# Kernel optimization log

Measured on AMD Instinct MI355X. Metric: run time of the kernel, lower is better.

## Reference

```python
import jax, jax.numpy as jnp
import numpy as np


def _log_g(x):
    # log of g(x) = where(x>=0, x+0.5, sigmoid(x)), computed stably in log space
    return jnp.where(x >= 0.0, jnp.log(jax.nn.relu(x) + 0.5), -jax.nn.softplus(-x))


def setup_inputs() -> dict:
    key = jax.random.key(0)
    k1, k2, k3, k4 = jax.random.split(key, 4)
    B, T, D, H = 4, 8192, 512, 512
    x = jax.random.normal(k1, (B, T, D), dtype=jnp.float32)
    h_prev = jax.random.uniform(k2, (B, 1, H), dtype=jnp.float32)  # positive: log(h0) taken
    W_h = jax.random.normal(k3, (H, D), dtype=jnp.float32) * (1.0 / np.sqrt(D))
    b_h = jnp.zeros((H,), dtype=jnp.float32)
    W_z = jax.random.normal(k4, (H, D), dtype=jnp.float32) * (1.0 / np.sqrt(D))
    b_z = jnp.zeros((H,), dtype=jnp.float32)
    return {"x": x, "h_prev": h_prev, "W_h": W_h, "b_h": b_h, "W_z": W_z, "b_z": b_z}


def reference(x, h_prev, W_h, b_h, W_z, b_z):
    # parallel (seq_len > 1) minGRU forward via Heinsen log-space scan
    k = jnp.einsum('btd,hd->bth', x, W_z) + b_z           # (B,T,H) gate pre-activation
    log_z = -jax.nn.softplus(-k)                          # log sigmoid(k)
    log_coeffs = -jax.nn.softplus(k)                      # log (1 - sigmoid(k))
    log_tilde_h = _log_g(jnp.einsum('btd,hd->bth', x, W_h) + b_h)
    log_h0 = jnp.log(h_prev)                              # (B,1,H)
    log_values = jnp.concatenate([log_h0, log_z + log_tilde_h], axis=1)  # (B,T+1,H)
    # a_star = [0, cumsum(log_coeffs)]
    a_star = jnp.pad(jnp.cumsum(log_coeffs, axis=1), ((0, 0), (1, 0), (0, 0)))
    log_h = a_star + jax.lax.cumlogsumexp(log_values - a_star, axis=1)
    h = jnp.exp(log_h)[:, 1:]                             # drop h0 -> (B,T,H)
    return h
```

## Files before the change

### kernel.cpp

```cpp
#include <hip/hip_runtime.h>
#include <hip/hip_bf16.h>
#include <stdint.h>

#define B_ 4
#define T_ 8192
#define D_ 512
#define H_ 512
#define M_ (B_ * T_)
#define SEG 32
#define SPB 256
#define NSEG (M_ / SEG)

typedef __attribute__((ext_vector_type(8))) short short8;
typedef __attribute__((ext_vector_type(4))) float floatx4;
typedef __attribute__((ext_vector_type(2))) float float2e;

__device__ __forceinline__ unsigned short f2bf(float f) {
    union { float f; unsigned int u; } v; v.f = f;
    unsigned int u = v.u;
    u += 0x7fffu + ((u >> 16) & 1u);
    return (unsigned short)(u >> 16);
}
__device__ __forceinline__ float bf_lo(unsigned int u) {
    union { unsigned int i; float f; } a; a.i = u << 16; return a.f;
}
__device__ __forceinline__ float bf_hi(unsigned int u) {
    union { unsigned int i; float f; } a; a.i = u & 0xffff0000u; return a.f;
}
__device__ __forceinline__ unsigned int pk_cd(float c, float d) {
    return (unsigned int)f2bf(c) | ((unsigned int)f2bf(d) << 16);
}

#define X8 (M_ * D_ / 8)
#define W8 (H_ * D_ / 8)

__global__ __launch_bounds__(256)
void conv_all(const float* __restrict__ x,
              const float* __restrict__ Wz,
              const float* __restrict__ Wh,
              unsigned short* __restrict__ xbf,
              unsigned short* __restrict__ Wf)
{
    const int gid    = blockIdx.x * blockDim.x + threadIdx.x;
    const int stride = gridDim.x * blockDim.x;
    for (int i = gid; i < X8; i += stride) {
        floatx4 a = __builtin_nontemporal_load((const floatx4*)x + 2 * i);
        floatx4 b = __builtin_nontemporal_load((const floatx4*)x + 2 * i + 1);
        short8 w;
        w[0] = (short)f2bf(a[0]); w[1] = (short)f2bf(a[1]);
        w[2] = (short)f2bf(a[2]); w[3] = (short)f2bf(a[3]);
        w[4] = (short)f2bf(b[0]); w[5] = (short)f2bf(b[1]);
        w[6] = (short)f2bf(b[2]); w[7] = (short)f2bf(b[3]);
        *((short8*)xbf + i) = w;
    }
    if (gid < 2 * W8) {
        const int i = gid;
        const float* src = (i < W8) ? Wz : Wh;
        const int idx = (i < W8) ? i : i - W8;
        floatx4 a = __builtin_nontemporal_load((const floatx4*)src + 2 * idx);
        floatx4 b = __builtin_nontemporal_load((const floatx4*)src + 2 * idx + 1);
        short8 w;
        w[0] = (short)f2bf(a[0]); w[1] = (short)f2bf(a[1]);
        w[2] = (short)f2bf(a[2]); w[3] = (short)f2bf(a[3]);
        w[4] = (short)f2bf(b[0]); w[5] = (short)f2bf(b[1]);
        w[6] = (short)f2bf(b[2]); w[7] = (short)f2bf(b[3]);
        *((short8*)Wf + i) = w;
    }
}

#define LDSB 32768

__global__ __launch_bounds__(256, 4)
void gemm_cd(const unsigned short* __restrict__ xbf,
             const unsigned short* __restrict__ Wf,
             const float* __restrict__ bz, const float* __restrict__ bh,
             unsigned int* __restrict__ cd,
             float2* __restrict__ Sagg)
{
    __shared__ __align__(16) char smem[LDSB];
    unsigned short* lds = (unsigned short*)smem;
    unsigned int*   cdl = (unsigned int*)smem;

    const int tid  = threadIdx.x;
    const int lane = tid & 63;
    const int wave = tid >> 6;
    const int xcd  = blockIdx.x & 7;
    const int nblk = (blockIdx.x >> 3) & 7;
    const int mblk = xcd * 32 + (blockIdx.x >> 6);
    const int m0 = mblk * 128;
    const int n0 = nblk * 64;
    const int wm = (wave >> 1) * 64;
    const int wn = (wave & 1) * 32;
    const int l15  = lane & 15;
    const int quad = lane >> 4;
    const int srow = lane >> 2;
    const int sp   = lane & 3;

    #define STAGE(p, kt)                                                          \
    {                                                                             \
        const int kb = (kt) * 32;                                                 \
        unsigned short* bb = lds + (p) * 8192;                                    \
        _Pragma("unroll")                                                         \
        for (int r = 0; r < 2; ++r) {                                             \
            const int chunk = r * 4 + wave;                                       \
            const int row   = chunk * 16 + srow;                                  \
            const int kp    = sp ^ (row & 3);                                     \
            __builtin_amdgcn_global_load_lds(                                     \
                (const __attribute__((address_space(1))) unsigned int*)           \
                    (xbf + (size_t)(m0 + row) * D_ + kb + kp * 8),                \
                (__attribute__((address_space(3))) unsigned int*)(bb + chunk * 512),\
                16, 0, 0);                                                        \
        }                                                                         \
        {                                                                         \
            const int row = wave * 16 + srow;                                     \
            const int kp  = sp ^ (row & 3);                                       \
            __builtin_amdgcn_global_load_lds(                                     \
                (const __attribute__((address_space(1))) unsigned int*)           \
                    (Wf + (size_t)(n0 + row) * D_ + kb + kp * 8),                 \
                (__attribute__((address_space(3))) unsigned int*)(bb + 4096 + wave * 512),\
                16, 0, 0);                                                        \
            __builtin_amdgcn_global_load_lds(                                     \
                (const __attribute__((address_space(1))) unsigned int*)           \
                    (Wf + (size_t)(512 + n0 + row) * D_ + kb + kp * 8),           \
                (__attribute__((address_space(3))) unsigned int*)(bb + 6144 + wave * 512),\
                16, 0, 0);                                                        \
        }                                                                         \
    }

    floatx4 acc_z[4][2], acc_h[4][2];
    #pragma unroll
    for (int i = 0; i < 4; ++i)
        #pragma unroll
        for (int j = 0; j < 2; ++j) { acc_z[i][j] = (floatx4)0.0f; acc_h[i][j] = (floatx4)0.0f; }

    STAGE(0, 0);

    for (int kt = 0; kt < 16; ++kt) {
        __syncthreads();
        const int base = (kt & 1) * 8192;
        short8 af[4], zf[2], hf[2];
        #pragma unroll
        for (int i = 0; i < 4; ++i) {
            const int ra = wm + i * 16 + l15;
            af[i] = *(const short8*)&lds[base + ra * 32 + ((quad ^ (ra & 3)) * 8)];
        }
        #pragma unroll
        for (int j = 0; j < 2; ++j) {
            const int rb = wn + j * 16 + l15;
            zf[j] = *(const short8*)&lds[base + 4096 + rb * 32 + ((quad ^ (rb & 3)) * 8)];
            hf[j] = *(const short8*)&lds[base + 6144 + rb * 32 + ((quad ^ (rb & 3)) * 8)];
        }
        if (kt < 15) STAGE((kt + 1) & 1, kt + 1);
        #pragma unroll
        for (int i = 0; i < 4; ++i)
            #pragma unroll
            for (int j = 0; j < 2; ++j) {
                acc_z[i][j] = __builtin_amdgcn_mfma_f32_16x16x32_bf16(zf[j], af[i], acc_z[i][j], 0, 0, 0);
                acc_h[i][j] = __builtin_amdgcn_mfma_f32_16x16x32_bf16(hf[j], af[i], acc_h[i][j], 0, 0, 0);
            }
    }

    __syncthreads();

    #pragma unroll
    for (int j = 0; j < 2; ++j) {
        const int hlb = wn + j * 16 + quad * 4;
        const float4 bzv = *(const float4*)&bz[n0 + hlb];
        const float4 bhv = *(const float4*)&bh[n0 + hlb];
        #pragma unroll
        for (int i = 0; i < 4; ++i) {
            const int mloc = wm + i * 16 + l15;
            uint4 w;
            #pragma unroll
            for (int r = 0; r < 4; ++r) {
                float kz = acc_z[i][j][r] + ((const float*)&bzv)[r];
                float hp = acc_h[i][j][r] + ((const float*)&bhv)[r];
                float c  = 1.0f / (1.0f + __expf(kz));
                float g  = (hp >= 0.0f) ? (hp + 0.5f) : (1.0f / (1.0f + __expf(-hp)));
                float d  = (1.0f - c) * g;
                ((unsigned int*)&w)[r] = pk_cd(c, d);
            }
            *(uint4*)&cd[(size_t)(m0 + mloc) * H_ + n0 + hlb] = w;
            *(uint4*)&cdl[mloc * 64 + (hlb ^ ((mloc & 7) << 2))] = w;
        }
    }

    __syncthreads();

    {
        float C = 1.0f, Dv = 0.0f;
        const int t0 = wave * 32;
        #pragma unroll
        for (int t = 0; t < 32; ++t) {
            const int row = t0 + t;
            unsigned int u = cdl[row * 64 + (lane ^ ((row & 7) << 2))];
            float c = bf_lo(u), d = bf_hi(u);
            Dv = fmaf(c, Dv, d);
            C *= c;
        }
        const int chain = (m0 >> 13) * 512 + n0 + lane;
        const int seg   = ((m0 >> 5) & 255) + wave;
        Sagg[(size_t)chain * SPB + seg] = make_float2(C, Dv);
    }
    #undef STAGE
}

__global__ __launch_bounds__(256)
void interseg(const float* __restrict__ h_prev,
              const float2* __restrict__ Sagg,
              float* __restrict__ Hseg)
{
    const int chain = blockIdx.x * 4 + (threadIdx.x >> 6);
    const int lane  = threadIdx.x & 63;
    const float2* spp = Sagg + (size_t)chain * SPB + lane * 4;
    float4 q0 = *(const float4*)&spp[0];
    float4 q1 = *(const float4*)&spp[2];
    float C = q0.x, D = q0.y;
    D = fmaf(q0.z, D, q0.w);  C *= q0.z;
    D = fmaf(q1.x, D, q1.y);  C *= q1.x;
    D = fmaf(q1.z, D, q1.w);  C *= q1.z;
    #pragma unroll
    for (int off = 1; off < 64; off <<= 1) {
        float Cp = __shfl_up(C, off, 64);
        float Dp = __shfl_up(D, off, 64);
        if (lane >= off) { D = fmaf(C, Dp, D); C *= Cp; }
    }
    float Ce = __shfl_up(C, 1, 64);
    float De = __shfl_up(D, 1, 64);
    if (lane == 0) { Ce = 1.0f; De = 0.0f; }
    const float h0 = h_prev[chain];
    float hs = fmaf(Ce, h0, De);
    float4 o;
    o.x = hs;
    hs = fmaf(q0.x, hs, q0.y); o.y = hs;
    hs = fmaf(q0.z, hs, q0.w); o.z = hs;
    hs = fmaf(q1.x, hs, q1.y); o.w = hs;
    *(float4*)&Hseg[(size_t)chain * SPB + lane * 4] = o;
}

__global__ __launch_bounds__(256)
void apply_scan(const unsigned int* __restrict__ cd,
                const float* __restrict__ Hseg,
                float* __restrict__ out)
{
    const int sg = blockIdx.x;
    const int b  = sg >> 8;
    const int s  = sg & 255;
    const int h  = threadIdx.x * 2;
    const unsigned int* base = cd + (size_t)sg * SEG * H_ + h;
    float* ob = out + (size_t)sg * SEG * H_ + h;
    uint2 v[SEG];
    #pragma unroll
    for (int t = 0; t < SEG; ++t)
        v[t] = *(const uint2*)(base + (size_t)t * H_);
    float hs0 = Hseg[(size_t)(b * 512 + h)     * SPB + s];
    float hs1 = Hseg[(size_t)(b * 512 + h + 1) * SPB + s];
    #pragma unroll
    for (int t = 0; t < SEG; ++t) {
        hs0 = fmaf(bf_lo(v[t].x), hs0, bf_hi(v[t].x));
        hs1 = fmaf(bf_lo(v[t].y), hs1, bf_hi(v[t].y));
        float2e o; o.x = hs0; o.y = hs1;
        __builtin_nontemporal_store(o, (float2e*)(ob + (size_t)t * H_));
    }
}

extern "C" void kernel_launch(void* const* d_in, const int* in_sizes, int n_in,
                              void* d_out, int out_size, void* d_ws, size_t ws_size,
                              hipStream_t stream)
{
    const float* x      = (const float*)d_in[0];
    const float* h_prev = (const float*)d_in[1];
    const float* W_h    = (const float*)d_in[2];
    const float* b_h    = (const float*)d_in[3];
    const float* W_z    = (const float*)d_in[4];
    const float* b_z    = (const float*)d_in[5];
    float* out = (float*)d_out;

    unsigned short* xbf = (unsigned short*)d_out;

    char* ws = (char*)d_ws;
    unsigned int* cd = (unsigned int*)ws;
    size_t cd_bytes = (size_t)M_ * H_ * 4;
    unsigned short* Wf = (unsigned short*)(ws + cd_bytes);
    size_t wf_bytes = (size_t)2 * H_ * D_ * sizeof(unsigned short);
    float2* Sagg = (float2*)(ws + cd_bytes + wf_bytes);
    float*  Hseg = (float*)((char*)Sagg + (size_t)2048 * SPB * sizeof(float2));

    conv_all<<<dim3(2048), dim3(256), 0, stream>>>(x, W_z, W_h, xbf, Wf);
    gemm_cd<<<dim3((M_ / 128) * (H_ / 64)), dim3(256), 0, stream>>>(
        xbf, Wf, b_z, b_h, cd, Sagg);
    interseg<<<dim3(512), dim3(256), 0, stream>>>(h_prev, Sagg, Hseg);
    apply_scan<<<dim3(NSEG), dim3(256), 0, stream>>>(cd, Hseg, out);
}
```

Before: 197.9 us.

## Triple-buffer GEMM K-loop, add nontemporal stores, widen apply_scan to 4 channels

The GEMM main loop moves from double to triple buffering in LDS, keeping two stages in flight. It replaces __syncthreads with explicit vmcnt waits and s_barrier, and unrolls the loop fully. The larger LDS footprint lowers the occupancy bound from 4 to 3 blocks. Stores of cd, Sagg and Hseg become nontemporal, and apply_scan now handles 4 channels per thread with 128-bit loads and stores, two segments per block, streaming loads instead of preloading all 32 rows into registers.

```diff
diff --git a/kernel.cpp b/kernel.cpp
--- a/kernel.cpp
+++ b/kernel.cpp
@@ -14,6 +14,7 @@
 typedef __attribute__((ext_vector_type(8))) short short8;
 typedef __attribute__((ext_vector_type(4))) float floatx4;
 typedef __attribute__((ext_vector_type(2))) float float2e;
+typedef __attribute__((ext_vector_type(4))) unsigned int uintx4;
 
 __device__ __forceinline__ unsigned short f2bf(float f) {
     union { float f; unsigned int u; } v; v.f = f;
@@ -68,9 +69,9 @@
     }
 }
 
-#define LDSB 32768
-
-__global__ __launch_bounds__(256, 4)
+#define LDSB 49152
+
+__global__ __launch_bounds__(256, 3)
 void gemm_cd(const unsigned short* __restrict__ xbf,
              const unsigned short* __restrict__ Wf,
              const float* __restrict__ bz, const float* __restrict__ bh,
@@ -134,10 +135,15 @@
         for (int j = 0; j < 2; ++j) { acc_z[i][j] = (floatx4)0.0f; acc_h[i][j] = (floatx4)0.0f; }
 
     STAGE(0, 0);
-
+    STAGE(1, 1);
+    __builtin_amdgcn_sched_barrier(0);
+    asm volatile("s_waitcnt vmcnt(4)" ::: "memory");
+    __builtin_amdgcn_s_barrier();
+    __builtin_amdgcn_sched_barrier(0);
+
+    #pragma unroll
     for (int kt = 0; kt < 16; ++kt) {
-        __syncthreads();
-        const int base = (kt & 1) * 8192;
+        const int base = (kt % 3) * 8192;
         short8 af[4], zf[2], hf[2];
         #pragma unroll
         for (int i = 0; i < 4; ++i) {
@@ -150,7 +156,7 @@
             zf[j] = *(const short8*)&lds[base + 4096 + rb * 32 + ((quad ^ (rb & 3)) * 8)];
             hf[j] = *(const short8*)&lds[base + 6144 + rb * 32 + ((quad ^ (rb & 3)) * 8)];
         }
-        if (kt < 15) STAGE((kt + 1) & 1, kt + 1);
+        if (kt <= 13) STAGE((kt + 2) % 3, kt + 2);
         #pragma unroll
         for (int i = 0; i < 4; ++i)
             #pragma unroll
@@ -158,6 +164,13 @@
                 acc_z[i][j] = __builtin_amdgcn_mfma_f32_16x16x32_bf16(zf[j], af[i], acc_z[i][j], 0, 0, 0);
                 acc_h[i][j] = __builtin_amdgcn_mfma_f32_16x16x32_bf16(hf[j], af[i], acc_h[i][j], 0, 0, 0);
             }
+        if (kt < 15) {
+            __builtin_amdgcn_sched_barrier(0);
+            if (kt <= 13) asm volatile("s_waitcnt vmcnt(4)" ::: "memory");
+            else          asm volatile("s_waitcnt vmcnt(0)" ::: "memory");
+            __builtin_amdgcn_s_barrier();
+            __builtin_amdgcn_sched_barrier(0);
+        }
     }
 
     __syncthreads();
@@ -170,7 +183,7 @@
         #pragma unroll
         for (int i = 0; i < 4; ++i) {
             const int mloc = wm + i * 16 + l15;
-            uint4 w;
+            uintx4 w;
             #pragma unroll
             for (int r = 0; r < 4; ++r) {
                 float kz = acc_z[i][j][r] + ((const float*)&bzv)[r];
@@ -178,10 +191,11 @@
                 float c  = 1.0f / (1.0f + __expf(kz));
                 float g  = (hp >= 0.0f) ? (hp + 0.5f) : (1.0f / (1.0f + __expf(-hp)));
                 float d  = (1.0f - c) * g;
-                ((unsigned int*)&w)[r] = pk_cd(c, d);
+                w[r] = pk_cd(c, d);
             }
-            *(uint4*)&cd[(size_t)(m0 + mloc) * H_ + n0 + hlb] = w;
-            *(uint4*)&cdl[mloc * 64 + (hlb ^ ((mloc & 7) << 2))] = w;
+            __builtin_nontemporal_store(w,
+                (uintx4*)&cd[(size_t)(m0 + mloc) * H_ + n0 + hlb]);
+            *(uintx4*)&cdl[mloc * 64 + (hlb ^ ((mloc & 7) << 2))] = w;
         }
     }
 
@@ -200,7 +214,8 @@
         }
         const int chain = (m0 >> 13) * 512 + n0 + lane;
         const int seg   = ((m0 >> 5) & 255) + wave;
-        Sagg[(size_t)chain * SPB + seg] = make_float2(C, Dv);
+        float2e sv; sv.x = C; sv.y = Dv;
+        __builtin_nontemporal_store(sv, (float2e*)&Sagg[(size_t)chain * SPB + seg]);
     }
     #undef STAGE
 }
@@ -230,12 +245,12 @@
     if (lane == 0) { Ce = 1.0f; De = 0.0f; }
     const float h0 = h_prev[chain];
     float hs = fmaf(Ce, h0, De);
-    float4 o;
-    o.x = hs;
-    hs = fmaf(q0.x, hs, q0.y); o.y = hs;
-    hs = fmaf(q0.z, hs, q0.w); o.z = hs;
-    hs = fmaf(q1.x, hs, q1.y); o.w = hs;
-    *(float4*)&Hseg[(size_t)chain * SPB + lane * 4] = o;
+    floatx4 o;
+    o[0] = hs;
+    hs = fmaf(q0.x, hs, q0.y); o[1] = hs;
+    hs = fmaf(q0.z, hs, q0.w); o[2] = hs;
+    hs = fmaf(q1.x, hs, q1.y); o[3] = hs;
+    __builtin_nontemporal_store(o, (floatx4*)&Hseg[(size_t)chain * SPB + lane * 4]);
 }
 
 __global__ __launch_bounds__(256)
@@ -243,24 +258,25 @@
                 const float* __restrict__ Hseg,
                 float* __restrict__ out)
 {
-    const int sg = blockIdx.x;
+    const int sg = blockIdx.x * 2 + (threadIdx.x >> 7);
     const int b  = sg >> 8;
     const int s  = sg & 255;
-    const int h  = threadIdx.x * 2;
+    const int h  = (threadIdx.x & 127) * 4;
+    float hs0 = Hseg[(size_t)(b * 512 + h)     * SPB + s];
+    float hs1 = Hseg[(size_t)(b * 512 + h + 1) * SPB + s];
+    float hs2 = Hseg[(size_t)(b * 512 + h + 2) * SPB + s];
+    float hs3 = Hseg[(size_t)(b * 512 + h + 3) * SPB + s];
     const unsigned int* base = cd + (size_t)sg * SEG * H_ + h;
     float* ob = out + (size_t)sg * SEG * H_ + h;
-    uint2 v[SEG];
-    #pragma unroll
-    for (int t = 0; t < SEG; ++t)
-        v[t] = *(const uint2*)(base + (size_t)t * H_);
-    float hs0 = Hseg[(size_t)(b * 512 + h)     * SPB + s];
-    float hs1 = Hseg[(size_t)(b * 512 + h + 1) * SPB + s];
     #pragma unroll
     for (int t = 0; t < SEG; ++t) {
-        hs0 = fmaf(bf_lo(v[t].x), hs0, bf_hi(v[t].x));
-        hs1 = fmaf(bf_lo(v[t].y), hs1, bf_hi(v[t].y));
-        float2e o; o.x = hs0; o.y = hs1;
-        __builtin_nontemporal_store(o, (float2e*)(ob + (size_t)t * H_));
+        uintx4 v = *(const uintx4*)(base + (size_t)t * H_);
+        hs0 = fmaf(bf_lo(v[0]), hs0, bf_hi(v[0]));
+        hs1 = fmaf(bf_lo(v[1]), hs1, bf_hi(v[1]));
+        hs2 = fmaf(bf_lo(v[2]), hs2, bf_hi(v[2]));
+        hs3 = fmaf(bf_lo(v[3]), hs3, bf_hi(v[3]));
+        floatx4 o; o[0] = hs0; o[1] = hs1; o[2] = hs2; o[3] = hs3;
+        __builtin_nontemporal_store(o, (floatx4*)(ob + (size_t)t * H_));
     }
 }
 
@@ -290,5 +306,5 @@
     gemm_cd<<<dim3((M_ / 128) * (H_ / 64)), dim3(256), 0, stream>>>(
         xbf, Wf, b_z, b_h, cd, Sagg);
     interseg<<<dim3(512), dim3(256), 0, stream>>>(h_prev, Sagg, Hseg);
-    apply_scan<<<dim3(NSEG), dim3(256), 0, stream>>>(cd, Hseg, out);
-}
+    apply_scan<<<dim3(NSEG / 2), dim3(256), 0, stream>>>(cd, Hseg, out);
+}
```

New measurement: 204.2 us. 3.2% more time.
